# Optimization experiments

Hardware: AMD Instinct MI355X
Metric: run time of the kernel (lower is better)

## Reference

```python
import jax, jax.numpy as jnp
import numpy as np

N_NODES = 50000
N_EDGES = 800000
F_IN = 32
HID = 64
K = 4  # Chebyshev order in GConvLSTM(node_features, hidden, 4)


def setup_inputs() -> dict:
    key = jax.random.key(0)
    ks = jax.random.split(key, 14)
    x = jax.random.normal(ks[0], (N_NODES, F_IN), dtype=jnp.float32)
    edge_index = jax.random.randint(ks[1], (2, N_EDGES), 0, N_NODES, dtype=jnp.int64)
    edge_weight = jax.random.uniform(ks[2], (N_EDGES,), dtype=jnp.float32)
    s = 0.05
    # gate order: i, f, c, o
    Wx = jax.random.normal(ks[3], (4, K, F_IN, HID), dtype=jnp.float32) * s  # ChebConv weights on x
    bx = jax.random.normal(ks[4], (4, HID), dtype=jnp.float32) * s          # ChebConv biases on x
    Wh = jax.random.normal(ks[5], (4, K, HID, HID), dtype=jnp.float32) * s  # ChebConv weights on h
    bh = jax.random.normal(ks[6], (4, HID), dtype=jnp.float32) * s          # ChebConv biases on h
    wc = jax.random.normal(ks[7], (3, HID), dtype=jnp.float32) * s          # peephole w_c_i, w_c_f, w_c_o
    bg = jax.random.normal(ks[8], (4, HID), dtype=jnp.float32) * s          # gate biases b_i, b_f, b_c, b_o
    lin_w = jax.random.normal(ks[9], (HID, 1), dtype=jnp.float32) * s
    lin_b = jax.random.normal(ks[10], (1,), dtype=jnp.float32) * s
    return {"x": x, "edge_index": edge_index, "edge_weight": edge_weight,
            "Wx": Wx, "bx": bx, "Wh": Wh, "bh": bh, "wc": wc, "bg": bg,
            "lin_w": lin_w, "lin_b": lin_b}


def _cheb_norm(edge_index, edge_weight, num_nodes):
    # ChebConv.__norm__, sym normalization, lambda_max=2.0:
    # L_hat off-diagonal = -D^{-1/2} A D^{-1/2}, diagonal = 0.
    src, dst = edge_index[0], edge_index[1]
    deg = jax.ops.segment_sum(edge_weight, src, num_segments=num_nodes)
    d_inv_sqrt = jnp.where(deg > 0, jax.lax.rsqrt(jnp.maximum(deg, 1e-30)), 0.0)
    norm = -d_inv_sqrt[src] * edge_weight * d_inv_sqrt[dst]
    return src, dst, norm


def _cheb_conv(v, src, dst, norm, W, b, num_nodes):
    # ChebConv forward: out = sum_k T_k(L_hat) v @ W[k] + b, with propagate
    # = segment_sum of norm * v[src] at dst.
    def prop(t):
        return jax.ops.segment_sum(norm[:, None] * t[src], dst, num_segments=num_nodes)
    Tx0 = v
    out = Tx0 @ W[0]
    Tx1 = prop(Tx0)
    out = out + Tx1 @ W[1]
    for k in range(2, W.shape[0]):
        Tx2 = 2.0 * prop(Tx1) - Tx0
        out = out + Tx2 @ W[k]
        Tx0, Tx1 = Tx1, Tx2
    return out + b


def reference(x, edge_index, edge_weight, Wx, bx, Wh, bh, wc, bg, lin_w, lin_b):
    N = x.shape[0]
    src, dst, norm = _cheb_norm(edge_index, edge_weight, N)
    H = jnp.zeros((N, Wh.shape[-1]), dtype=x.dtype)
    C = jnp.zeros((N, Wh.shape[-1]), dtype=x.dtype)

    def gate(g, v_state):
        return (_cheb_conv(x, src, dst, norm, Wx[g], bx[g], N)
                + _cheb_conv(v_state, src, dst, norm, Wh[g], bh[g], N))

    I = jax.nn.sigmoid(gate(0, H) + wc[0] * C + bg[0])
    F = jax.nn.sigmoid(gate(1, H) + wc[1] * C + bg[1])
    T = jnp.tanh(gate(2, H) + bg[2])
    C = F * C + I * T
    O = jax.nn.sigmoid(gate(3, H) + wc[2] * C + bg[3])
    H = O * jnp.tanh(C)
    # dropout(p=0.25) is identity at inference; linear head HID -> 1
    return H @ lin_w + lin_b
```

## Files before the change

### kernel.cpp

```cpp
#include <hip/hip_runtime.h>
#include <math.h>


#define NT 256
#define RS 8192
#define NCH 32

typedef __attribute__((ext_vector_type(8))) short short8v;
typedef __attribute__((ext_vector_type(8))) unsigned short ushort8v;
typedef __attribute__((ext_vector_type(4))) float f32x4;

__device__ __forceinline__ short f2bf(float f) {
    unsigned u = __float_as_uint(f);
    u += 0x7FFFu + ((u >> 16) & 1u);
    return (short)(u >> 16);
}
__device__ __forceinline__ float bf2f(unsigned short b) {
    return __uint_as_float((unsigned)b << 16);
}

__global__ __launch_bounds__(1024)
void k_hist(const int* __restrict__ src, const int* __restrict__ dst,
            const float* __restrict__ w, float* __restrict__ degPart,
            int* __restrict__ cntPart, int nE, int N) {
    __shared__ float s_deg[RS];
    __shared__ int   s_cnt[RS];
    const int r = blockIdx.x / NCH, b = blockIdx.x % NCH;
    const int base = r * RS;
    for (int i = threadIdx.x; i < RS; i += 1024) { s_deg[i] = 0.f; s_cnt[i] = 0; }
    __syncthreads();
    const int chunk = (nE + NCH - 1) / NCH;
    const int e0 = b * chunk, e1 = min(e0 + chunk, nE);
    for (int e = e0 + (int)threadIdx.x; e < e1; e += 1024) {
        int s = src[e], d = dst[e];
        unsigned so = (unsigned)(s - base), dof = (unsigned)(d - base);
        if (so < RS) atomicAdd(&s_deg[so], w[e]);
        if (dof < RS) atomicAdd(&s_cnt[dof], 1);
    }
    __syncthreads();
    for (int i = threadIdx.x; i < RS; i += 1024) {
        int n = base + i;
        if (n < N) {
            degPart[(size_t)b * N + n] = s_deg[i];
            cntPart[(size_t)b * N + n] = s_cnt[i];
        }
    }
}

__global__ __launch_bounds__(NT)
void k_reduce_scanA(const float* __restrict__ degPart, const int* __restrict__ cntPart,
                    float* __restrict__ dinv, int* __restrict__ cnt,
                    int* __restrict__ rowptr, int* __restrict__ partials, int N) {
    __shared__ int s[NT];
    int t = threadIdx.x, i = blockIdx.x * NT + t;
    int c = 0;
    if (i < N) {
        float d = 0.f;
#pragma unroll
        for (int b = 0; b < NCH; ++b) {
            d += degPart[(size_t)b * N + i];
            c += cntPart[(size_t)b * N + i];
        }
        dinv[i] = d > 0.f ? rsqrtf(d) : 0.f;
        cnt[i] = c;
    }
    s[t] = c;
    __syncthreads();
    for (int off = 1; off < NT; off <<= 1) {
        int u = (t >= off) ? s[t - off] : 0;
        __syncthreads();
        s[t] += u;
        __syncthreads();
    }
    if (i < N) rowptr[i] = s[t] - c;
    if (t == NT - 1) partials[blockIdx.x] = s[t];
}

__global__ void k_scanB(int* __restrict__ partials, int nb) {
    __shared__ int s[1024];
    int t = threadIdx.x;
    int v = (t < nb) ? partials[t] : 0;
    s[t] = v;
    __syncthreads();
    for (int off = 1; off < 1024; off <<= 1) {
        int u = (t >= off) ? s[t - off] : 0;
        __syncthreads();
        s[t] += u;
        __syncthreads();
    }
    if (t < nb) partials[t] = s[t] - v;
}

__global__ void k_scanC_off(int* __restrict__ rowptr, const int* __restrict__ partials,
                            int* __restrict__ cntPart, int N) {
    int n = blockIdx.x * NT + threadIdx.x;
    if (n >= N) return;
    int v = rowptr[n] + partials[blockIdx.x];
    rowptr[n] = v;
    int s = v;
#pragma unroll
    for (int b = 0; b < NCH; ++b) {
        int t = cntPart[(size_t)b * N + n];
        cntPart[(size_t)b * N + n] = s;
        s += t;
    }
}

__global__ __launch_bounds__(1024)
void k_fill2(const int* __restrict__ src, const int* __restrict__ dst,
             const float* __restrict__ w, const float* __restrict__ dinv,
             const int* __restrict__ offs, int2* __restrict__ entries,
             int nE, int N) {
    __shared__ int s_cur[RS];
    const int r = blockIdx.x / NCH, b = blockIdx.x % NCH;
    const int base = r * RS;
    for (int i = threadIdx.x; i < RS; i += 1024) {
        int n = base + i;
        s_cur[i] = (n < N) ? offs[(size_t)b * N + n] : 0;
    }
    __syncthreads();
    const int chunk = (nE + NCH - 1) / NCH;
    const int e0 = b * chunk, e1 = min(e0 + chunk, nE);
    for (int e = e0 + (int)threadIdx.x; e < e1; e += 1024) {
        int d = dst[e];
        unsigned dof = (unsigned)(d - base);
        if (dof < RS) {
            int s = src[e];
            float nv = -dinv[s] * w[e] * dinv[d];
            int pos = atomicAdd(&s_cur[dof], 1);
            entries[pos] = make_int2(s, __float_as_int(nv));
        }
    }
}

__device__ __forceinline__ void bf8_fma(float* acc, ushort8v v, float s) {
#pragma unroll
    for (int j = 0; j < 8; ++j)
        acc[j] = fmaf(s, bf2f(v[j]), acc[j]);
}

__global__ __launch_bounds__(256)
void k_gather_bf(const unsigned short* __restrict__ tb,
                 const float* __restrict__ subf,
                 const unsigned short* __restrict__ subb,
                 short* __restrict__ outb,
                 const int* __restrict__ rowptr, const int* __restrict__ cnt,
                 const int2* __restrict__ entries, float scale, int N) {
    int idx = blockIdx.x * blockDim.x + threadIdx.x;
    if (idx >= N * 4) return;
    int n = idx >> 2, q = idx & 3;
    int beg = rowptr[n], end = beg + cnt[n];
    float acc0[8] = {0, 0, 0, 0, 0, 0, 0, 0};
    float acc1[8] = {0, 0, 0, 0, 0, 0, 0, 0};
    int i = beg;
    for (; i + 3 < end; i += 4) {
        int2 e0 = entries[i];
        int2 e1 = entries[i + 1];
        int2 e2 = entries[i + 2];
        int2 e3 = entries[i + 3];
        ushort8v v0 = *reinterpret_cast<const ushort8v*>(tb + (size_t)e0.x * 32 + q * 8);
        ushort8v v1 = *reinterpret_cast<const ushort8v*>(tb + (size_t)e1.x * 32 + q * 8);
        ushort8v v2 = *reinterpret_cast<const ushort8v*>(tb + (size_t)e2.x * 32 + q * 8);
        ushort8v v3 = *reinterpret_cast<const ushort8v*>(tb + (size_t)e3.x * 32 + q * 8);
        bf8_fma(acc0, v0, __int_as_float(e0.y));
        bf8_fma(acc1, v1, __int_as_float(e1.y));
        bf8_fma(acc0, v2, __int_as_float(e2.y));
        bf8_fma(acc1, v3, __int_as_float(e3.y));
    }
    for (; i < end; ++i) {
        int2 e0 = entries[i];
        ushort8v v0 = *reinterpret_cast<const ushort8v*>(tb + (size_t)e0.x * 32 + q * 8);
        bf8_fma(acc0, v0, __int_as_float(e0.y));
    }
    float r[8];
#pragma unroll
    for (int j = 0; j < 8; ++j) r[j] = scale * (acc0[j] + acc1[j]);
    if (subf) {
#pragma unroll
        for (int j = 0; j < 8; ++j) r[j] -= subf[(size_t)n * 32 + q * 8 + j];
    } else if (subb) {
        ushort8v sv = *reinterpret_cast<const ushort8v*>(subb + (size_t)n * 32 + q * 8);
#pragma unroll
        for (int j = 0; j < 8; ++j) r[j] -= bf2f(sv[j]);
    }
    short8v rb;
#pragma unroll
    for (int j = 0; j < 8; ++j) rb[j] = f2bf(r[j]);
    *reinterpret_cast<short8v*>(outb + (size_t)n * 32 + q * 8) = rb;
}

__global__ void k_xb(const float* __restrict__ x, short* __restrict__ xb, int n4) {
    int i = blockIdx.x * blockDim.x + threadIdx.x;
    if (i >= n4) return;
    const float4 v = *reinterpret_cast<const float4*>(x + (size_t)i * 4);
    short4 rb;
    rb.x = f2bf(v.x); rb.y = f2bf(v.y); rb.z = f2bf(v.z); rb.w = f2bf(v.w);
    *reinterpret_cast<short4*>(xb + (size_t)i * 4) = rb;
}

__global__ void k_prepack(const float* __restrict__ Wx, short* __restrict__ P) {
    int t = blockIdx.x * blockDim.x + threadIdx.x;
    if (t >= 12 * 4 * 64) return;
    int lane = t & 63;
    int kt = (t >> 6) & 3;
    int nt = t >> 8;
    int gate = (nt < 4) ? 0 : (nt < 8) ? 2 : 3;
    int h = (nt & 3) * 16 + (lane & 15);
    int fb = (lane >> 4) * 8;
    short8v v;
#pragma unroll
    for (int j = 0; j < 8; ++j)
        v[j] = f2bf(Wx[((size_t)(gate * 4 + kt) * 32 + fb + j) * 64 + h]);
    *(reinterpret_cast<short8v*>(P) + t) = v;
}

__device__ __forceinline__ float sigf(float x) {
    return __builtin_amdgcn_rcpf(1.f + __builtin_amdgcn_exp2f(-1.4426950408889634f * x));
}
__device__ __forceinline__ float tanhf_fast(float x) {
    float e = __builtin_amdgcn_exp2f(2.8853900817779268f * x);
    return 1.f - 2.f * __builtin_amdgcn_rcpf(e + 1.f);
}

__global__ __launch_bounds__(256)
void k_final_mfma(const short* __restrict__ xb, const short* __restrict__ t1b,
                  const short* __restrict__ t2b, const short* __restrict__ t3b,
                  const short* __restrict__ P, const float* __restrict__ bx,
                  const float* __restrict__ bh, const float* __restrict__ wc,
                  const float* __restrict__ bg, const float* __restrict__ lin_w,
                  const float* __restrict__ lin_b, float* __restrict__ out, int N) {
    const int wave = threadIdx.x >> 6, lane = threadIdx.x & 63;
    const int nb = blockIdx.x * 64 + wave * 16;
    const int rc = min(nb + (lane & 15), N - 1);
    const int ko = (lane >> 4) * 8;

    short8v A0 = *reinterpret_cast<const short8v*>(xb  + (size_t)rc * 32 + ko);
    short8v A1 = *reinterpret_cast<const short8v*>(t1b + (size_t)rc * 32 + ko);
    short8v A2 = *reinterpret_cast<const short8v*>(t2b + (size_t)rc * 32 + ko);
    short8v A3 = *reinterpret_cast<const short8v*>(t3b + (size_t)rc * 32 + ko);

    const short8v* Pv = reinterpret_cast<const short8v*>(P);
    f32x4 acc[12];
#pragma unroll
    for (int nt = 0; nt < 12; ++nt) {
        const short8v* Pb = Pv + (size_t)nt * 4 * 64 + lane;
        f32x4 a = {0.f, 0.f, 0.f, 0.f};
        a = __builtin_amdgcn_mfma_f32_16x16x32_bf16(A0, Pb[0],   a, 0, 0, 0);
        a = __builtin_amdgcn_mfma_f32_16x16x32_bf16(A1, Pb[64],  a, 0, 0, 0);
        a = __builtin_amdgcn_mfma_f32_16x16x32_bf16(A2, Pb[128], a, 0, 0, 0);
        a = __builtin_amdgcn_mfma_f32_16x16x32_bf16(A3, Pb[192], a, 0, 0, 0);
        acc[nt] = a;
    }

    const int hq = lane & 15;
    const int ng = lane >> 4;
    const float lb = lin_b[0];
    float p[4] = {0.f, 0.f, 0.f, 0.f};
#pragma unroll
    for (int ht = 0; ht < 4; ++ht) {
        int h = ht * 16 + hq;
        float bI = bx[h] + bh[h] + bg[h];
        float bC = bx[128 + h] + bh[128 + h] + bg[128 + h];
        float bO = bx[192 + h] + bh[192 + h] + bg[192 + h];
        float w2 = wc[128 + h];
        float lw = lin_w[h];
#pragma unroll
        for (int r = 0; r < 4; ++r) {
            float I = sigf(acc[ht][r] + bI);
            float T = tanhf_fast(acc[4 + ht][r] + bC);
            float C = I * T;
            float O = sigf(acc[8 + ht][r] + bO + w2 * C);
            float H = O * tanhf_fast(C);
            p[r] = fmaf(H, lw, p[r]);
        }
    }
#pragma unroll
    for (int r = 0; r < 4; ++r) {
        float v = p[r];
        v += __shfl_xor(v, 1);
        v += __shfl_xor(v, 2);
        v += __shfl_xor(v, 4);
        v += __shfl_xor(v, 8);
        if (hq == 0) {
            int n = nb + ng * 4 + r;
            if (n < N) out[n] = v + lb;
        }
    }
}

extern "C" void kernel_launch(void* const* d_in, const int* in_sizes, int n_in,
                              void* d_out, int out_size, void* d_ws, size_t ws_size,
                              hipStream_t stream) {
    const float* x   = (const float*)d_in[0];
    const int*   ei  = (const int*)d_in[1];
    const float* ew  = (const float*)d_in[2];
    const float* Wx  = (const float*)d_in[3];
    const float* bx  = (const float*)d_in[4];
    const float* bh  = (const float*)d_in[6];
    const float* wcp = (const float*)d_in[7];
    const float* bg  = (const float*)d_in[8];
    const float* lw  = (const float*)d_in[9];
    const float* lb  = (const float*)d_in[10];
    float* out = (float*)d_out;

    const int N  = in_sizes[0] / 32;
    const int nE = in_sizes[2];
    const int* src = ei;
    const int* dst = ei + nE;

    char* ws = (char*)d_ws;
    size_t off = 0;
    float* dinv    = (float*)(ws + off); off += (size_t)N * 4;
    int*   cnt     = (int*)(ws + off);   off += (size_t)N * 4;
    int*   rowptr  = (int*)(ws + off);   off += (size_t)N * 4;
    int*   partials= (int*)(ws + off);   off += 1024 * 4;
    short* P       = (short*)(ws + off); off += 12 * 4 * 64 * 8 * 2;
    int2*  entries = (int2*)(ws + off);  off += (size_t)nE * 8;
    float* degPart = (float*)(ws + off); off += (size_t)NCH * N * 4;
    int*   cntPart = (int*)(ws + off);   off += (size_t)NCH * N * 4;
    short* xbuf    = (short*)(ws + off); off += (size_t)N * 32 * 2;
    short* Tx1b    = (short*)(ws + off); off += (size_t)N * 32 * 2;
    short* Tx2b    = (short*)(ws + off); off += (size_t)N * 32 * 2;
    short* Tx3b    = (short*)(ws + off); off += (size_t)N * 32 * 2;

    const int nb = (N + NT - 1) / NT;
    const int nRange = (N + RS - 1) / RS;

    k_hist<<<nRange * NCH, 1024, 0, stream>>>(src, dst, ew, degPart, cntPart, nE, N);
    k_prepack<<<(12 * 4 * 64 + NT - 1) / NT, NT, 0, stream>>>(Wx, P);
    k_xb<<<(N * 8 + NT - 1) / NT, NT, 0, stream>>>(x, xbuf, N * 8);
    k_reduce_scanA<<<nb, NT, 0, stream>>>(degPart, cntPart, dinv, cnt, rowptr,
                                          partials, N);
    k_scanB<<<1, 1024, 0, stream>>>(partials, nb);
    k_scanC_off<<<nb, NT, 0, stream>>>(rowptr, partials, cntPart, N);
    k_fill2<<<nRange * NCH, 1024, 0, stream>>>(src, dst, ew, dinv, cntPart,
                                               entries, nE, N);

    const int gb = (N * 4 + NT - 1) / NT;
    k_gather_bf<<<gb, NT, 0, stream>>>((const unsigned short*)xbuf, nullptr, nullptr,
                                       Tx1b, rowptr, cnt, entries, 1.f, N);
    k_gather_bf<<<gb, NT, 0, stream>>>((const unsigned short*)Tx1b, x, nullptr,
                                       Tx2b, rowptr, cnt, entries, 2.f, N);
    k_gather_bf<<<gb, NT, 0, stream>>>((const unsigned short*)Tx2b, nullptr,
                                       (const unsigned short*)Tx1b,
                                       Tx3b, rowptr, cnt, entries, 2.f, N);

    const int fb = (N + 63) / 64;
    k_final_mfma<<<fb, NT, 0, stream>>>(xbuf, Tx1b, Tx2b, Tx3b, P, bx, bh, wcp,
                                        bg, lw, lb, out, N);
}
```

Before: 119.0 us.

## Fuse third Chebyshev gather into MFMA epilogue and split gather rows across lanes

The third sparse propagation (Tx3) is now computed inside the final MFMA kernel, which removes one launch and the write and re-read of the Tx3 buffer. The standalone gather now gives each row to 8 threads, two halves that each take alternating edges and combine with a shuffle, to get more memory parallelism. The histogram and fill kernels use 16K-node shared-memory ranges so fewer blocks each rescan the edge list. Weight prepacking and x-to-bf16 conversion are merged into one launch, and Tx2 now subtracts the bf16 copy of x instead of the fp32 x. Risks: the fused gather in the final kernel runs with only 16 rows per wave, and the larger shared arrays reduce occupancy.

```diff
diff --git a/kernel.cpp b/kernel.cpp
--- a/kernel.cpp
+++ b/kernel.cpp
@@ -3,7 +3,8 @@
 
 
 #define NT 256
-#define RS 8192
+#define RSH 16384
+#define RSF 16384
 #define NCH 32
 
 typedef __attribute__((ext_vector_type(8))) short short8v;
@@ -23,27 +24,25 @@
 void k_hist(const int* __restrict__ src, const int* __restrict__ dst,
             const float* __restrict__ w, float* __restrict__ degPart,
             int* __restrict__ cntPart, int nE, int N) {
-    __shared__ float s_deg[RS];
-    __shared__ int   s_cnt[RS];
+    __shared__ float s_deg[RSH];
+    __shared__ int   s_cnt[RSH];
     const int r = blockIdx.x / NCH, b = blockIdx.x % NCH;
-    const int base = r * RS;
-    for (int i = threadIdx.x; i < RS; i += 1024) { s_deg[i] = 0.f; s_cnt[i] = 0; }
+    const int base = r * RSH;
+    for (int i = threadIdx.x; i < RSH; i += 1024) { s_deg[i] = 0.f; s_cnt[i] = 0; }
     __syncthreads();
     const int chunk = (nE + NCH - 1) / NCH;
     const int e0 = b * chunk, e1 = min(e0 + chunk, nE);
     for (int e = e0 + (int)threadIdx.x; e < e1; e += 1024) {
         int s = src[e], d = dst[e];
         unsigned so = (unsigned)(s - base), dof = (unsigned)(d - base);
-        if (so < RS) atomicAdd(&s_deg[so], w[e]);
-        if (dof < RS) atomicAdd(&s_cnt[dof], 1);
-    }
-    __syncthreads();
-    for (int i = threadIdx.x; i < RS; i += 1024) {
-        int n = base + i;
-        if (n < N) {
-            degPart[(size_t)b * N + n] = s_deg[i];
-            cntPart[(size_t)b * N + n] = s_cnt[i];
-        }
+        if (so < RSH) atomicAdd(&s_deg[so], w[e]);
+        if (dof < RSH) atomicAdd(&s_cnt[dof], 1);
+    }
+    __syncthreads();
+    const int lim = min(RSH, N - base);
+    for (int i = threadIdx.x; i < lim; i += 1024) {
+        degPart[(size_t)b * N + base + i] = s_deg[i];
+        cntPart[(size_t)b * N + base + i] = s_cnt[i];
     }
 }
 
@@ -111,20 +110,19 @@
              const float* __restrict__ w, const float* __restrict__ dinv,
              const int* __restrict__ offs, int2* __restrict__ entries,
              int nE, int N) {
-    __shared__ int s_cur[RS];
+    __shared__ int s_cur[RSF];
     const int r = blockIdx.x / NCH, b = blockIdx.x % NCH;
-    const int base = r * RS;
-    for (int i = threadIdx.x; i < RS; i += 1024) {
-        int n = base + i;
-        s_cur[i] = (n < N) ? offs[(size_t)b * N + n] : 0;
-    }
+    const int base = r * RSF;
+    const int lim = min(RSF, N - base);
+    for (int i = threadIdx.x; i < lim; i += 1024)
+        s_cur[i] = offs[(size_t)b * N + base + i];
     __syncthreads();
     const int chunk = (nE + NCH - 1) / NCH;
     const int e0 = b * chunk, e1 = min(e0 + chunk, nE);
     for (int e = e0 + (int)threadIdx.x; e < e1; e += 1024) {
         int d = dst[e];
         unsigned dof = (unsigned)(d - base);
-        if (dof < RS) {
+        if (dof < RSF) {
             int s = src[e];
             float nv = -dinv[s] * w[e] * dinv[d];
             int pos = atomicAdd(&s_cur[dof], 1);
@@ -141,15 +139,108 @@
 
 __global__ __launch_bounds__(256)
 void k_gather_bf(const unsigned short* __restrict__ tb,
-                 const float* __restrict__ subf,
                  const unsigned short* __restrict__ subb,
                  short* __restrict__ outb,
                  const int* __restrict__ rowptr, const int* __restrict__ cnt,
                  const int2* __restrict__ entries, float scale, int N) {
     int idx = blockIdx.x * blockDim.x + threadIdx.x;
-    if (idx >= N * 4) return;
-    int n = idx >> 2, q = idx & 3;
+    if (idx >= N * 8) return;
+    int n = idx >> 3, tq = idx & 3, half = (idx >> 2) & 1;
     int beg = rowptr[n], end = beg + cnt[n];
+    float acc0[8] = {0, 0, 0, 0, 0, 0, 0, 0};
+    float acc1[8] = {0, 0, 0, 0, 0, 0, 0, 0};
+    int i = beg + half;
+    for (; i + 6 < end; i += 8) {
+        int2 e0 = entries[i];
+        int2 e1 = entries[i + 2];
+        int2 e2 = entries[i + 4];
+        int2 e3 = entries[i + 6];
+        ushort8v v0 = *reinterpret_cast<const ushort8v*>(tb + (size_t)e0.x * 32 + tq * 8);
+        ushort8v v1 = *reinterpret_cast<const ushort8v*>(tb + (size_t)e1.x * 32 + tq * 8);
+        ushort8v v2 = *reinterpret_cast<const ushort8v*>(tb + (size_t)e2.x * 32 + tq * 8);
+        ushort8v v3 = *reinterpret_cast<const ushort8v*>(tb + (size_t)e3.x * 32 + tq * 8);
+        bf8_fma(acc0, v0, __int_as_float(e0.y));
+        bf8_fma(acc1, v1, __int_as_float(e1.y));
+        bf8_fma(acc0, v2, __int_as_float(e2.y));
+        bf8_fma(acc1, v3, __int_as_float(e3.y));
+    }
+    for (; i < end; i += 2) {
+        int2 e0 = entries[i];
+        ushort8v v0 = *reinterpret_cast<const ushort8v*>(tb + (size_t)e0.x * 32 + tq * 8);
+        bf8_fma(acc0, v0, __int_as_float(e0.y));
+    }
+    float r[8];
+#pragma unroll
+    for (int j = 0; j < 8; ++j) {
+        r[j] = acc0[j] + acc1[j];
+        r[j] += __shfl_xor(r[j], 4);
+    }
+    if (!half) {
+        if (subb) {
+            ushort8v sv = *reinterpret_cast<const ushort8v*>(subb + (size_t)n * 32 + tq * 8);
+#pragma unroll
+            for (int j = 0; j < 8; ++j) r[j] = fmaf(scale, r[j], -bf2f(sv[j]));
+        } else {
+#pragma unroll
+            for (int j = 0; j < 8; ++j) r[j] *= scale;
+        }
+        short8v rb;
+#pragma unroll
+        for (int j = 0; j < 8; ++j) rb[j] = f2bf(r[j]);
+        *reinterpret_cast<short8v*>(outb + (size_t)n * 32 + tq * 8) = rb;
+    }
+}
+
+__global__ void k_prepack_xb(const float* __restrict__ Wx, short* __restrict__ P,
+                             const float* __restrict__ x, short* __restrict__ xb,
+                             int n4) {
+    int idx = blockIdx.x * blockDim.x + threadIdx.x;
+    if (idx < 12 * 4 * 64) {
+        int lane = idx & 63;
+        int kt = (idx >> 6) & 3;
+        int nt = idx >> 8;
+        int gate = (nt < 4) ? 0 : (nt < 8) ? 2 : 3;
+        int h = (nt & 3) * 16 + (lane & 15);
+        int fb = (lane >> 4) * 8;
+        short8v v;
+#pragma unroll
+        for (int j = 0; j < 8; ++j)
+            v[j] = f2bf(Wx[((size_t)(gate * 4 + kt) * 32 + fb + j) * 64 + h]);
+        *(reinterpret_cast<short8v*>(P) + idx) = v;
+        return;
+    }
+    int i = idx - 12 * 4 * 64;
+    if (i >= n4) return;
+    const float4 v = *reinterpret_cast<const float4*>(x + (size_t)i * 4);
+    short4 rb;
+    rb.x = f2bf(v.x); rb.y = f2bf(v.y); rb.z = f2bf(v.z); rb.w = f2bf(v.w);
+    *reinterpret_cast<short4*>(xb + (size_t)i * 4) = rb;
+}
+
+__device__ __forceinline__ float sigf(float x) {
+    return __builtin_amdgcn_rcpf(1.f + __builtin_amdgcn_exp2f(-1.4426950408889634f * x));
+}
+__device__ __forceinline__ float tanhf_fast(float x) {
+    float e = __builtin_amdgcn_exp2f(2.8853900817779268f * x);
+    return 1.f - 2.f * __builtin_amdgcn_rcpf(e + 1.f);
+}
+
+__global__ __launch_bounds__(256)
+void k_final_g3(const short* __restrict__ xb, const short* __restrict__ t1b,
+                const unsigned short* __restrict__ t2b,
+                const short* __restrict__ P,
+                const int* __restrict__ rowptr, const int* __restrict__ cnt,
+                const int2* __restrict__ entries,
+                const float* __restrict__ bx, const float* __restrict__ bh,
+                const float* __restrict__ wc, const float* __restrict__ bg,
+                const float* __restrict__ lin_w, const float* __restrict__ lin_b,
+                float* __restrict__ out, int N) {
+    const int wave = threadIdx.x >> 6, lane = threadIdx.x & 63;
+    const int nb = blockIdx.x * 64 + wave * 16;
+    const int rc = min(nb + (lane & 15), N - 1);
+    const int ko = (lane >> 4) * 8;
+
+    int beg = rowptr[rc], end = beg + cnt[rc];
     float acc0[8] = {0, 0, 0, 0, 0, 0, 0, 0};
     float acc1[8] = {0, 0, 0, 0, 0, 0, 0, 0};
     int i = beg;
@@ -158,10 +249,10 @@
         int2 e1 = entries[i + 1];
         int2 e2 = entries[i + 2];
         int2 e3 = entries[i + 3];
-        ushort8v v0 = *reinterpret_cast<const ushort8v*>(tb + (size_t)e0.x * 32 + q * 8);
-        ushort8v v1 = *reinterpret_cast<const ushort8v*>(tb + (size_t)e1.x * 32 + q * 8);
-        ushort8v v2 = *reinterpret_cast<const ushort8v*>(tb + (size_t)e2.x * 32 + q * 8);
-        ushort8v v3 = *reinterpret_cast<const ushort8v*>(tb + (size_t)e3.x * 32 + q * 8);
+        ushort8v v0 = *reinterpret_cast<const ushort8v*>(t2b + (size_t)e0.x * 32 + ko);
+        ushort8v v1 = *reinterpret_cast<const ushort8v*>(t2b + (size_t)e1.x * 32 + ko);
+        ushort8v v2 = *reinterpret_cast<const ushort8v*>(t2b + (size_t)e2.x * 32 + ko);
+        ushort8v v3 = *reinterpret_cast<const ushort8v*>(t2b + (size_t)e3.x * 32 + ko);
         bf8_fma(acc0, v0, __int_as_float(e0.y));
         bf8_fma(acc1, v1, __int_as_float(e1.y));
         bf8_fma(acc0, v2, __int_as_float(e2.y));
@@ -169,75 +260,18 @@
     }
     for (; i < end; ++i) {
         int2 e0 = entries[i];
-        ushort8v v0 = *reinterpret_cast<const ushort8v*>(tb + (size_t)e0.x * 32 + q * 8);
+        ushort8v v0 = *reinterpret_cast<const ushort8v*>(t2b + (size_t)e0.x * 32 + ko);
         bf8_fma(acc0, v0, __int_as_float(e0.y));
     }
-    float r[8];
-#pragma unroll
-    for (int j = 0; j < 8; ++j) r[j] = scale * (acc0[j] + acc1[j]);
-    if (subf) {
-#pragma unroll
-        for (int j = 0; j < 8; ++j) r[j] -= subf[(size_t)n * 32 + q * 8 + j];
-    } else if (subb) {
-        ushort8v sv = *reinterpret_cast<const ushort8v*>(subb + (size_t)n * 32 + q * 8);
-#pragma unroll
-        for (int j = 0; j < 8; ++j) r[j] -= bf2f(sv[j]);
-    }
-    short8v rb;
-#pragma unroll
-    for (int j = 0; j < 8; ++j) rb[j] = f2bf(r[j]);
-    *reinterpret_cast<short8v*>(outb + (size_t)n * 32 + q * 8) = rb;
-}
-
-__global__ void k_xb(const float* __restrict__ x, short* __restrict__ xb, int n4) {
-    int i = blockIdx.x * blockDim.x + threadIdx.x;
-    if (i >= n4) return;
-    const float4 v = *reinterpret_cast<const float4*>(x + (size_t)i * 4);
-    short4 rb;
-    rb.x = f2bf(v.x); rb.y = f2bf(v.y); rb.z = f2bf(v.z); rb.w = f2bf(v.w);
-    *reinterpret_cast<short4*>(xb + (size_t)i * 4) = rb;
-}
-
-__global__ void k_prepack(const float* __restrict__ Wx, short* __restrict__ P) {
-    int t = blockIdx.x * blockDim.x + threadIdx.x;
-    if (t >= 12 * 4 * 64) return;
-    int lane = t & 63;
-    int kt = (t >> 6) & 3;
-    int nt = t >> 8;
-    int gate = (nt < 4) ? 0 : (nt < 8) ? 2 : 3;
-    int h = (nt & 3) * 16 + (lane & 15);
-    int fb = (lane >> 4) * 8;
-    short8v v;
-#pragma unroll
-    for (int j = 0; j < 8; ++j)
-        v[j] = f2bf(Wx[((size_t)(gate * 4 + kt) * 32 + fb + j) * 64 + h]);
-    *(reinterpret_cast<short8v*>(P) + t) = v;
-}
-
-__device__ __forceinline__ float sigf(float x) {
-    return __builtin_amdgcn_rcpf(1.f + __builtin_amdgcn_exp2f(-1.4426950408889634f * x));
-}
-__device__ __forceinline__ float tanhf_fast(float x) {
-    float e = __builtin_amdgcn_exp2f(2.8853900817779268f * x);
-    return 1.f - 2.f * __builtin_amdgcn_rcpf(e + 1.f);
-}
-
-__global__ __launch_bounds__(256)
-void k_final_mfma(const short* __restrict__ xb, const short* __restrict__ t1b,
-                  const short* __restrict__ t2b, const short* __restrict__ t3b,
-                  const short* __restrict__ P, const float* __restrict__ bx,
-                  const float* __restrict__ bh, const float* __restrict__ wc,
-                  const float* __restrict__ bg, const float* __restrict__ lin_w,
-                  const float* __restrict__ lin_b, float* __restrict__ out, int N) {
-    const int wave = threadIdx.x >> 6, lane = threadIdx.x & 63;
-    const int nb = blockIdx.x * 64 + wave * 16;
-    const int rc = min(nb + (lane & 15), N - 1);
-    const int ko = (lane >> 4) * 8;
 
     short8v A0 = *reinterpret_cast<const short8v*>(xb  + (size_t)rc * 32 + ko);
     short8v A1 = *reinterpret_cast<const short8v*>(t1b + (size_t)rc * 32 + ko);
-    short8v A2 = *reinterpret_cast<const short8v*>(t2b + (size_t)rc * 32 + ko);
-    short8v A3 = *reinterpret_cast<const short8v*>(t3b + (size_t)rc * 32 + ko);
+    short8v A2 = *reinterpret_cast<const short8v*>(
+        reinterpret_cast<const short*>(t2b) + (size_t)rc * 32 + ko);
+    short8v A3;
+#pragma unroll
+    for (int j = 0; j < 8; ++j)
+        A3[j] = f2bf(2.f * (acc0[j] + acc1[j]) - bf2f((unsigned short)A1[j]));
 
     const short8v* Pv = reinterpret_cast<const short8v*>(P);
     f32x4 acc[12];
@@ -321,31 +355,29 @@
     short* xbuf    = (short*)(ws + off); off += (size_t)N * 32 * 2;
     short* Tx1b    = (short*)(ws + off); off += (size_t)N * 32 * 2;
     short* Tx2b    = (short*)(ws + off); off += (size_t)N * 32 * 2;
-    short* Tx3b    = (short*)(ws + off); off += (size_t)N * 32 * 2;
 
     const int nb = (N + NT - 1) / NT;
-    const int nRange = (N + RS - 1) / RS;
-
-    k_hist<<<nRange * NCH, 1024, 0, stream>>>(src, dst, ew, degPart, cntPart, nE, N);
-    k_prepack<<<(12 * 4 * 64 + NT - 1) / NT, NT, 0, stream>>>(Wx, P);
-    k_xb<<<(N * 8 + NT - 1) / NT, NT, 0, stream>>>(x, xbuf, N * 8);
+    const int nRangeH = (N + RSH - 1) / RSH;
+    const int nRangeF = (N + RSF - 1) / RSF;
+
+    k_hist<<<nRangeH * NCH, 1024, 0, stream>>>(src, dst, ew, degPart, cntPart, nE, N);
+    k_prepack_xb<<<(12 * 4 * 64 + N * 8 + NT - 1) / NT, NT, 0, stream>>>(Wx, P, x, xbuf, N * 8);
     k_reduce_scanA<<<nb, NT, 0, stream>>>(degPart, cntPart, dinv, cnt, rowptr,
                                           partials, N);
     k_scanB<<<1, 1024, 0, stream>>>(partials, nb);
     k_scanC_off<<<nb, NT, 0, stream>>>(rowptr, partials, cntPart, N);
-    k_fill2<<<nRange * NCH, 1024, 0, stream>>>(src, dst, ew, dinv, cntPart,
-                                               entries, nE, N);
-
-    const int gb = (N * 4 + NT - 1) / NT;
-    k_gather_bf<<<gb, NT, 0, stream>>>((const unsigned short*)xbuf, nullptr, nullptr,
+    k_fill2<<<nRangeF * NCH, 1024, 0, stream>>>(src, dst, ew, dinv, cntPart,
+                                                entries, nE, N);
+
+    const int gb = (N * 8 + NT - 1) / NT;
+    k_gather_bf<<<gb, NT, 0, stream>>>((const unsigned short*)xbuf, nullptr,
                                        Tx1b, rowptr, cnt, entries, 1.f, N);
-    k_gather_bf<<<gb, NT, 0, stream>>>((const unsigned short*)Tx1b, x, nullptr,
+    k_gather_bf<<<gb, NT, 0, stream>>>((const unsigned short*)Tx1b,
+                                       (const unsigned short*)xbuf,
                                        Tx2b, rowptr, cnt, entries, 2.f, N);
-    k_gather_bf<<<gb, NT, 0, stream>>>((const unsigned short*)Tx2b, nullptr,
-                                       (const unsigned short*)Tx1b,
-                                       Tx3b, rowptr, cnt, entries, 2.f, N);
 
     const int fb = (N + 63) / 64;
-    k_final_mfma<<<fb, NT, 0, stream>>>(xbuf, Tx1b, Tx2b, Tx3b, P, bx, bh, wcp,
-                                        bg, lw, lb, out, N);
-}
+    k_final_g3<<<fb, NT, 0, stream>>>(xbuf, Tx1b, (const unsigned short*)Tx2b, P,
+                                      rowptr, cnt, entries, bx, bh, wcp, bg,
+                                      lw, lb, out, N);
+}
```

After: 118.3 us. No clear change (-0.6%).
